# Kernel tuning notes

Hardware: AMD Instinct MI355X
Metric: run time of the kernel (lower is better)

## Reference

```python
import jax, jax.numpy as jnp
import numpy as np

NUM_NODES = 50000
NUM_GRAPHS = 50
HID = 128
GFD = 2
L = 4
EPS_MSG = 1e-7


def layer_norm(x, g, b, eps=1e-5):
    mu = jnp.mean(x, axis=-1, keepdims=True)
    xc = x - mu
    var = jnp.mean(xc * xc, axis=-1, keepdims=True)
    return xc * jax.lax.rsqrt(var + eps) * g + b


def gen_conv(x, src, dst, ea, t, W1, b1, g1, be1, W2, b2):
    # GENConv message: relu(x_j + edge_attr) + eps  -> [E, h]
    msg = jax.nn.relu(x[src] + ea) + EPS_MSG
    # per-destination, per-channel softmax weights of t*msg
    logits = msg * t
    m = jax.ops.segment_max(logits, dst, num_segments=NUM_NODES)
    m = jnp.where(jnp.isfinite(m), m, 0.0)  # isolated nodes -> -inf guard
    m = jax.lax.stop_gradient(m)
    ex = jnp.exp(logits - m[dst])
    s = jax.ops.segment_sum(ex, dst, num_segments=NUM_NODES)
    agg = jax.ops.segment_sum(ex * msg, dst, num_segments=NUM_NODES) / jnp.where(s > 0, s, 1.0)
    out = agg + x  # root residual inside GENConv
    # GENConv MLP: Linear(h,2h) -> LayerNorm -> ReLU -> Linear(2h,h)
    h = layer_norm(out @ W1 + b1, g1, be1)
    h = jax.nn.relu(h)
    return h @ W2 + b2


def forward(x, edge_index, edge_attr, graph_features, node_W, node_b, edge_W, edge_b,
            ts, W1s, b1s, g1s, be1s, W2s, b2s, ln_gs, ln_bs,
            head_W0, head_b0, head_W1, head_b1):
    src, dst = edge_index[0], edge_index[1]
    x = x @ node_W + node_b                 # node_encoder
    ea = edge_attr @ edge_W + edge_b        # edge_encoder
    # layers[0].conv applied directly (no pre-norm)
    x = gen_conv(x, src, dst, ea, ts[0], W1s[0], b1s[0], g1s[0], be1s[0], W2s[0], b2s[0])
    # remaining layers: res+ blocks: x = x + conv(act(norm(x)))
    for i in range(1, L):
        h = jax.nn.relu(layer_norm(x, ln_gs[i], ln_bs[i]))
        h = gen_conv(h, src, dst, ea, ts[i], W1s[i], b1s[i], g1s[i], be1s[i], W2s[i], b2s[i])
        x = x + h
    # final norm/act taken from layers[0]
    x = jax.nn.relu(layer_norm(x, ln_gs[0], ln_bs[0]))
    # dropout(p=0.1) is identity in eval mode
    # graph features broadcast to nodes (faithful reshape sequence)
    G = graph_features.shape[0]
    npg = x.shape[0] // G                   # nodes per graph
    t = jnp.repeat(graph_features.T[:, :, None], npg, axis=2)  # [gfd, G, npg]
    t = t.reshape(G, GFD, npg)              # row-major reinterpret (torch .view)
    t = jnp.transpose(t, (1, 0, 2)).reshape(GFD, G * npg)      # cat(unbind(0), dim=1)
    x = jnp.concatenate([x, t.T], axis=1)   # [N, h + gfd]
    x = jax.nn.relu(x @ head_W0 + head_b0)
    x = x @ head_W1 + head_b1
    return x


def setup_inputs() -> dict:
    key = jax.random.key(0)
    ks = jax.random.split(key, 32)
    E = 800000
    d_in, d_e = 64, 16

    def lin(k, fi, fo):
        return jax.random.normal(k, (fi, fo), jnp.float32) / np.sqrt(fi)

    inp = {
        'x': jax.random.normal(ks[0], (NUM_NODES, d_in), jnp.float32),
        'edge_index': jax.random.randint(ks[1], (2, E), 0, NUM_NODES, jnp.int64 if jax.config.jax_enable_x64 else jnp.int32),
        'edge_attr': jax.random.normal(ks[2], (E, d_e), jnp.float32),
        'graph_features': jax.random.normal(ks[3], (NUM_GRAPHS, GFD), jnp.float32),
        'node_W': lin(ks[4], d_in, HID), 'node_b': jnp.zeros((HID,), jnp.float32),
        'edge_W': lin(ks[5], d_e, HID), 'edge_b': jnp.zeros((HID,), jnp.float32),
        'ts': jnp.ones((L,), jnp.float32),
        'W1s': jnp.stack([lin(ks[6 + i], HID, 2 * HID) for i in range(L)]),
        'b1s': jnp.zeros((L, 2 * HID), jnp.float32),
        'g1s': jnp.ones((L, 2 * HID), jnp.float32),
        'be1s': jnp.zeros((L, 2 * HID), jnp.float32),
        'W2s': jnp.stack([lin(ks[10 + i], 2 * HID, HID) for i in range(L)]),
        'b2s': jnp.zeros((L, HID), jnp.float32),
        'ln_gs': jnp.ones((L, HID), jnp.float32),
        'ln_bs': jnp.zeros((L, HID), jnp.float32),
        'head_W0': lin(ks[14], HID + GFD, HID), 'head_b0': jnp.zeros((HID,), jnp.float32),
        'head_W1': lin(ks[15], HID, 1), 'head_b1': jnp.zeros((1,), jnp.float32),
    }
    return inp


def reference(x, edge_index, edge_attr, graph_features, node_W, node_b, edge_W, edge_b,
              ts, W1s, b1s, g1s, be1s, W2s, b2s, ln_gs, ln_bs,
              head_W0, head_b0, head_W1, head_b1):
    return forward(x, edge_index, edge_attr, graph_features, node_W, node_b, edge_W, edge_b,
                   ts, W1s, b1s, g1s, be1s, W2s, b2s, ln_gs, ln_bs,
                   head_W0, head_b0, head_W1, head_b1)
```

## Files before the change

### kernel.cpp

```cpp
#include <hip/hip_runtime.h>
#include <math.h>

#define EPS_MSG 1e-7f

typedef float v2f __attribute__((ext_vector_type(2)));
typedef float v4f __attribute__((ext_vector_type(4)));
typedef short bf16x8 __attribute__((ext_vector_type(8)));
typedef float f32x4 __attribute__((ext_vector_type(4)));
typedef unsigned short ush;

static __device__ inline v2f sp(float a) { v2f r; r.x = a; r.y = a; return r; }

__device__ inline unsigned short f2bf(float f) {
    union { float f; unsigned int i; } u; u.f = f;
    unsigned int b = u.i;
    return (unsigned short)((b + 0x7fffu + ((b >> 16) & 1u)) >> 16);
}
__device__ inline float bf2f(unsigned short h) {
    union { unsigned int i; float f; } u; u.i = ((unsigned int)h) << 16;
    return u.f;
}

__global__ void zero2_kernel(int* __restrict__ a, int* __restrict__ b, int n) {
    int i = blockIdx.x * 256 + threadIdx.x;
    if (i < n) { a[i] = 0; b[i] = 0; }
}

__global__ void deg_kernel(const int* __restrict__ ei, int* __restrict__ deg, int E) {
    int e = blockIdx.x * 256 + threadIdx.x;
    if (e < E) atomicAdd(&deg[ei[E + e]], 1);
}

__global__ __launch_bounds__(1024)
void scan1_kernel(const int* __restrict__ deg, int* __restrict__ offs,
                  int* __restrict__ bsum, int n) {
    __shared__ int sh[1024];
    int tid = threadIdx.x;
    int i = blockIdx.x * 1024 + tid;
    int v = (i < n) ? deg[i] : 0;
    sh[tid] = v;
    __syncthreads();
    for (int off = 1; off < 1024; off <<= 1) {
        int t = (tid >= off) ? sh[tid - off] : 0;
        __syncthreads();
        sh[tid] += t;
        __syncthreads();
    }
    if (i < n) offs[i] = sh[tid] - v;
    if (tid == 1023) bsum[blockIdx.x] = sh[tid];
}

__global__ __launch_bounds__(64)
void scan2_kernel(int* __restrict__ bsum, int nb) {
    int lane = threadIdx.x;
    int carry = 0;
    for (int base = 0; base < nb; base += 64) {
        int v = (base + lane < nb) ? bsum[base + lane] : 0;
        int incl = v;
#pragma unroll
        for (int off = 1; off < 64; off <<= 1) {
            int t = __shfl_up(incl, off, 64);
            if (lane >= off) incl += t;
        }
        if (base + lane < nb) bsum[base + lane] = incl - v + carry;
        carry += __shfl(incl, 63, 64);
    }
    if (lane == 0) bsum[nb] = carry;
}

__global__ void scan3_kernel(int* __restrict__ offs, const int* __restrict__ bsum, int n) {
    int i = blockIdx.x * 256 + threadIdx.x;
    if (i < n) offs[i] += bsum[i >> 10];
    else if (i == n) offs[n] = bsum[(n + 1023) >> 10];
}

__global__ void scatter_kernel(const int* __restrict__ ei, const float* __restrict__ edge_attr,
                               const int* __restrict__ offs, int* __restrict__ fill,
                               int* __restrict__ src_perm, float* __restrict__ attr_perm, int E) {
    int e = blockIdx.x * 256 + threadIdx.x;
    if (e >= E) return;
    int s = ei[e];
    int d = ei[E + e];
    int pos = offs[d] + atomicAdd(&fill[d], 1);
    src_perm[pos] = s;
    const float4* a = (const float4*)&edge_attr[(size_t)e * 16];
    float4* b = (float4*)&attr_perm[(size_t)pos * 16];
    b[0] = a[0]; b[1] = a[1]; b[2] = a[2]; b[3] = a[3];
}

__global__ void wswz_kernel(const float* __restrict__ W, unsigned short* __restrict__ WH,
                            unsigned short* __restrict__ WL, int K, int Ncol, int total) {
    int idx = blockIdx.x * 256 + threadIdx.x;
    if (idx >= total) return;
    int j = idx & 7;
    int lane = (idx >> 3) & 63;
    int rest = idx >> 9;
    int ks = K >> 5;
    int kstep = rest % ks;
    int rest2 = rest / ks;
    int nc = Ncol >> 4;
    int c16 = rest2 % nc;
    int l = rest2 / nc;
    int k = kstep * 32 + (lane >> 4) * 8 + j;
    int n = c16 * 16 + (lane & 15);
    float v = W[(size_t)l * K * Ncol + (size_t)k * Ncol + n];
    unsigned short hi = f2bf(v);
    unsigned short lo = f2bf(v - bf2f(hi));
    WH[idx] = hi;
    WL[idx] = lo;
}

__global__ __launch_bounds__(256)
void encode_kernel(const float* __restrict__ x, const float* __restrict__ W,
                   const float* __restrict__ b, float* __restrict__ out, int N) {
    __shared__ __align__(16) float Xa[32][64];
    int tid = threadIdx.x;
    int node0 = blockIdx.x * 32;
    {
        int row = tid >> 3;
        int col = (tid & 7) * 8;
        float4 v0 = make_float4(0, 0, 0, 0), v1 = make_float4(0, 0, 0, 0);
        if (node0 + row < N) {
            const float* sp_ = &x[(size_t)(node0 + row) * 64 + col];
            v0 = *(const float4*)sp_;
            v1 = *(const float4*)(sp_ + 4);
        }
        *(float4*)&Xa[row][col] = v0;
        *(float4*)&Xa[row][col + 4] = v1;
    }
    __syncthreads();
    int tx = tid & 31, rg = tid >> 5;
    int c = tx * 4;
    v2f ba = *(const v2f*)&b[c];
    v2f bb = *(const v2f*)&b[c + 2];
    v2f acc[4][2];
#pragma unroll
    for (int i = 0; i < 4; ++i) { acc[i][0] = ba; acc[i][1] = bb; }
    for (int k = 0; k < 64; k += 4) {
        v4f W0 = *(const v4f*)&W[(k + 0) * 128 + c];
        v4f W1r = *(const v4f*)&W[(k + 1) * 128 + c];
        v4f W2r = *(const v4f*)&W[(k + 2) * 128 + c];
        v4f W3r = *(const v4f*)&W[(k + 3) * 128 + c];
#pragma unroll
        for (int i = 0; i < 4; ++i) {
            v4f xv = *(const v4f*)&Xa[rg * 4 + i][k];
            acc[i][0] = __builtin_elementwise_fma(sp(xv.x), W0.xy, acc[i][0]);
            acc[i][1] = __builtin_elementwise_fma(sp(xv.x), W0.zw, acc[i][1]);
            acc[i][0] = __builtin_elementwise_fma(sp(xv.y), W1r.xy, acc[i][0]);
            acc[i][1] = __builtin_elementwise_fma(sp(xv.y), W1r.zw, acc[i][1]);
            acc[i][0] = __builtin_elementwise_fma(sp(xv.z), W2r.xy, acc[i][0]);
            acc[i][1] = __builtin_elementwise_fma(sp(xv.z), W2r.zw, acc[i][1]);
            acc[i][0] = __builtin_elementwise_fma(sp(xv.w), W3r.xy, acc[i][0]);
            acc[i][1] = __builtin_elementwise_fma(sp(xv.w), W3r.zw, acc[i][1]);
        }
    }
#pragma unroll
    for (int i = 0; i < 4; ++i) {
        int row = node0 + rg * 4 + i;
        if (row < N) {
            float4 o = make_float4(acc[i][0].x, acc[i][0].y, acc[i][1].x, acc[i][1].y);
            *(float4*)&out[(size_t)row * 128 + c] = o;
        }
    }
}

__global__ __launch_bounds__(256)
void ln_relu_kernel(const float* __restrict__ x, const float* __restrict__ g,
                    const float* __restrict__ b, float* __restrict__ out, int N) {
    int lane = threadIdx.x & 63;
    int node = blockIdx.x * 4 + (threadIdx.x >> 6);
    if (node >= N) return;
    int c0 = lane * 2;
    float2 xv = *(const float2*)&x[(size_t)node * 128 + c0];
    float s = xv.x + xv.y;
    float q = xv.x * xv.x + xv.y * xv.y;
#pragma unroll
    for (int m = 1; m < 64; m <<= 1) { s += __shfl_xor(s, m, 64); q += __shfl_xor(q, m, 64); }
    float mu = s * (1.f / 128.f);
    float var = q * (1.f / 128.f) - mu * mu;
    float rs = rsqrtf(var + 1e-5f);
    float ox = fmaxf((xv.x - mu) * rs * g[c0] + b[c0], 0.f);
    float oy = fmaxf((xv.y - mu) * rs * g[c0 + 1] + b[c0 + 1], 0.f);
    float2 o; o.x = ox; o.y = oy;
    *(float2*)&out[(size_t)node * 128 + c0] = o;
}

__global__ __launch_bounds__(256)
void ln_relu_bf_kernel(const float* __restrict__ x, const float* __restrict__ g,
                       const float* __restrict__ b, unsigned short* __restrict__ outH,
                       unsigned short* __restrict__ outL, int N) {
    int lane = threadIdx.x & 63;
    int node = blockIdx.x * 4 + (threadIdx.x >> 6);
    if (node >= N) return;
    int c0 = lane * 2;
    float2 xv = *(const float2*)&x[(size_t)node * 128 + c0];
    float s = xv.x + xv.y;
    float q = xv.x * xv.x + xv.y * xv.y;
#pragma unroll
    for (int m = 1; m < 64; m <<= 1) { s += __shfl_xor(s, m, 64); q += __shfl_xor(q, m, 64); }
    float mu = s * (1.f / 128.f);
    float var = q * (1.f / 128.f) - mu * mu;
    float rs = rsqrtf(var + 1e-5f);
    float ox = fmaxf((xv.x - mu) * rs * g[c0] + b[c0], 0.f);
    float oy = fmaxf((xv.y - mu) * rs * g[c0 + 1] + b[c0 + 1], 0.f);
    unsigned short hx = f2bf(ox), hy = f2bf(oy);
    unsigned short lx = f2bf(ox - bf2f(hx)), ly = f2bf(oy - bf2f(hy));
    *(unsigned int*)&outH[(size_t)node * 128 + c0] = (unsigned int)hx | ((unsigned int)hy << 16);
    *(unsigned int*)&outL[(size_t)node * 128 + c0] = (unsigned int)lx | ((unsigned int)ly << 16);
}

__global__ __launch_bounds__(256, 4)
void conv_kernel(const float* __restrict__ pre, const float* __restrict__ attr_perm,
                 const int* __restrict__ src_perm, const int* __restrict__ offs,
                 const float* __restrict__ edge_W, const float* __restrict__ edge_b,
                 const float* __restrict__ ts, int layer,
                 unsigned short* __restrict__ convH, unsigned short* __restrict__ convL, int N) {
    int lane = threadIdx.x & 63;
    int node = blockIdx.x * 4 + (threadIdx.x >> 6);
    if (node >= N) return;
    int c0 = lane * 2;
    v2f wE[16];
#pragma unroll
    for (int k = 0; k < 16; ++k) {
        wE[k].x = edge_W[k * 128 + c0];
        wE[k].y = edge_W[k * 128 + c0 + 1];
    }
    v2f eb; eb.x = edge_b[c0]; eb.y = edge_b[c0 + 1];
    float t = ts[layer];
    int i0 = offs[node], i1 = offs[node + 1];
    v2f xself = *(const v2f*)&pre[(size_t)node * 128 + c0];
    float sx = 0.f, sy = 0.f, wx = 0.f, wy = 0.f;
    int i = i0;
    for (; i + 3 < i1; i += 4) {
        int iu = __builtin_amdgcn_readfirstlane(i);
        int sn0 = src_perm[iu];
        int sn1 = src_perm[iu + 1];
        int sn2 = src_perm[iu + 2];
        int sn3 = src_perm[iu + 3];
        v2f x0 = *(const v2f*)&pre[(size_t)sn0 * 128 + c0];
        v2f x1 = *(const v2f*)&pre[(size_t)sn1 * 128 + c0];
        v2f x2 = *(const v2f*)&pre[(size_t)sn2 * 128 + c0];
        v2f x3 = *(const v2f*)&pre[(size_t)sn3 * 128 + c0];
        const v4f* ar = (const v4f*)(attr_perm + (size_t)iu * 16);
        v2f ea0 = eb, ea1 = eb, ea2 = eb, ea3 = eb;
#pragma unroll
        for (int k = 0; k < 4; ++k) {
            v4f A0 = ar[k];
            v4f A1 = ar[4 + k];
            v4f A2 = ar[8 + k];
            v4f A3 = ar[12 + k];
            ea0 = __builtin_elementwise_fma(sp(A0.x), wE[4 * k + 0], ea0);
            ea1 = __builtin_elementwise_fma(sp(A1.x), wE[4 * k + 0], ea1);
            ea2 = __builtin_elementwise_fma(sp(A2.x), wE[4 * k + 0], ea2);
            ea3 = __builtin_elementwise_fma(sp(A3.x), wE[4 * k + 0], ea3);
            ea0 = __builtin_elementwise_fma(sp(A0.y), wE[4 * k + 1], ea0);
            ea1 = __builtin_elementwise_fma(sp(A1.y), wE[4 * k + 1], ea1);
            ea2 = __builtin_elementwise_fma(sp(A2.y), wE[4 * k + 1], ea2);
            ea3 = __builtin_elementwise_fma(sp(A3.y), wE[4 * k + 1], ea3);
            ea0 = __builtin_elementwise_fma(sp(A0.z), wE[4 * k + 2], ea0);
            ea1 = __builtin_elementwise_fma(sp(A1.z), wE[4 * k + 2], ea1);
            ea2 = __builtin_elementwise_fma(sp(A2.z), wE[4 * k + 2], ea2);
            ea3 = __builtin_elementwise_fma(sp(A3.z), wE[4 * k + 2], ea3);
            ea0 = __builtin_elementwise_fma(sp(A0.w), wE[4 * k + 3], ea0);
            ea1 = __builtin_elementwise_fma(sp(A1.w), wE[4 * k + 3], ea1);
            ea2 = __builtin_elementwise_fma(sp(A2.w), wE[4 * k + 3], ea2);
            ea3 = __builtin_elementwise_fma(sp(A3.w), wE[4 * k + 3], ea3);
        }
        float m0x = fmaxf(x0.x + ea0.x, 0.f) + EPS_MSG;
        float m0y = fmaxf(x0.y + ea0.y, 0.f) + EPS_MSG;
        float m1x = fmaxf(x1.x + ea1.x, 0.f) + EPS_MSG;
        float m1y = fmaxf(x1.y + ea1.y, 0.f) + EPS_MSG;
        float m2x = fmaxf(x2.x + ea2.x, 0.f) + EPS_MSG;
        float m2y = fmaxf(x2.y + ea2.y, 0.f) + EPS_MSG;
        float m3x = fmaxf(x3.x + ea3.x, 0.f) + EPS_MSG;
        float m3y = fmaxf(x3.y + ea3.y, 0.f) + EPS_MSG;
        float e0x = __expf(m0x * t), e0y = __expf(m0y * t);
        float e1x = __expf(m1x * t), e1y = __expf(m1y * t);
        float e2x = __expf(m2x * t), e2y = __expf(m2y * t);
        float e3x = __expf(m3x * t), e3y = __expf(m3y * t);
        sx += (e0x + e1x) + (e2x + e3x);
        sy += (e0y + e1y) + (e2y + e3y);
        wx = fmaf(e0x, m0x, wx); wx = fmaf(e1x, m1x, wx);
        wx = fmaf(e2x, m2x, wx); wx = fmaf(e3x, m3x, wx);
        wy = fmaf(e0y, m0y, wy); wy = fmaf(e1y, m1y, wy);
        wy = fmaf(e2y, m2y, wy); wy = fmaf(e3y, m3y, wy);
    }
    for (; i < i1; ++i) {
        int iu = __builtin_amdgcn_readfirstlane(i);
        int sn = src_perm[iu];
        const v4f* ar = (const v4f*)(attr_perm + (size_t)iu * 16);
        v2f xv = *(const v2f*)&pre[(size_t)sn * 128 + c0];
        v2f ea = eb;
#pragma unroll
        for (int k = 0; k < 4; ++k) {
            v4f A0 = ar[k];
            ea = __builtin_elementwise_fma(sp(A0.x), wE[4 * k + 0], ea);
            ea = __builtin_elementwise_fma(sp(A0.y), wE[4 * k + 1], ea);
            ea = __builtin_elementwise_fma(sp(A0.z), wE[4 * k + 2], ea);
            ea = __builtin_elementwise_fma(sp(A0.w), wE[4 * k + 3], ea);
        }
        float mgx = fmaxf(xv.x + ea.x, 0.f) + EPS_MSG;
        float mgy = fmaxf(xv.y + ea.y, 0.f) + EPS_MSG;
        float ex = __expf(mgx * t), ey = __expf(mgy * t);
        sx += ex; sy += ey;
        wx = fmaf(ex, mgx, wx);
        wy = fmaf(ey, mgy, wy);
    }
    float ax = (sx > 0.f) ? wx / sx : 0.f;
    float ay = (sy > 0.f) ? wy / sy : 0.f;
    float ox = ax + xself.x;
    float oy = ay + xself.y;
    unsigned short hx = f2bf(ox), hy = f2bf(oy);
    unsigned short lx = f2bf(ox - bf2f(hx)), ly = f2bf(oy - bf2f(hy));
    *(unsigned int*)&convH[(size_t)node * 128 + c0] = (unsigned int)hx | ((unsigned int)hy << 16);
    *(unsigned int*)&convL[(size_t)node * 128 + c0] = (unsigned int)lx | ((unsigned int)ly << 16);
}

template <int RES>
__global__ __launch_bounds__(256)
void mlp_mfma(const unsigned short* __restrict__ convH, const unsigned short* __restrict__ convL,
              const unsigned short* __restrict__ W1H, const unsigned short* __restrict__ W1L,
              const float* __restrict__ b1, const float* __restrict__ g1, const float* __restrict__ be1,
              const unsigned short* __restrict__ W2H, const unsigned short* __restrict__ W2L,
              const float* __restrict__ b2, const float* __restrict__ xold,
              float* __restrict__ xnew, int N) {
    __shared__ __align__(16) char SH[33792];
    __shared__ float2 ps[4][32];
    ush (*XaH)[136] = (ush(*)[136])&SH[0];
    ush (*XaL)[136] = (ush(*)[136])&SH[8704];
    ush (*XhH)[264] = (ush(*)[264])&SH[0];
    ush (*XhL)[264] = (ush(*)[264])&SH[16896];
    int tid = threadIdx.x;
    int w = tid >> 6;
    int lane = tid & 63;
    int g = lane >> 4;
    int r = lane & 15;
    int node0 = blockIdx.x * 32;
    {
        int row = tid >> 3;
        int cb = (tid & 7) * 16;
        uint4 h0 = make_uint4(0, 0, 0, 0), h1 = h0, l0 = h0, l1 = h0;
        if (node0 + row < N) {
            const uint4* pH = (const uint4*)&convH[(size_t)(node0 + row) * 128 + cb];
            const uint4* pL = (const uint4*)&convL[(size_t)(node0 + row) * 128 + cb];
            h0 = pH[0]; h1 = pH[1];
            l0 = pL[0]; l1 = pL[1];
        }
        *(uint4*)&XaH[row][cb] = h0; *(uint4*)&XaH[row][cb + 8] = h1;
        *(uint4*)&XaL[row][cb] = l0; *(uint4*)&XaL[row][cb + 8] = l1;
    }
    __syncthreads();
    f32x4 acc1[2][4];
#pragma unroll
    for (int cf = 0; cf < 4; ++cf) {
        float bv = b1[(w * 4 + cf) * 16 + r];
        f32x4 iv; iv[0] = bv; iv[1] = bv; iv[2] = bv; iv[3] = bv;
        acc1[0][cf] = iv; acc1[1][cf] = iv;
    }
#pragma unroll
    for (int kstep = 0; kstep < 4; ++kstep) {
        int ko = kstep * 32 + g * 8;
        bf16x8 aH0 = *(const bf16x8*)&XaH[r][ko];
        bf16x8 aH1 = *(const bf16x8*)&XaH[16 + r][ko];
        bf16x8 aL0 = *(const bf16x8*)&XaL[r][ko];
        bf16x8 aL1 = *(const bf16x8*)&XaL[16 + r][ko];
#pragma unroll
        for (int cf = 0; cf < 4; ++cf) {
            int c16 = w * 4 + cf;
            bf16x8 bH = *(const bf16x8*)&W1H[(((size_t)c16 * 4 + kstep) * 64 + lane) * 8];
            bf16x8 bL = *(const bf16x8*)&W1L[(((size_t)c16 * 4 + kstep) * 64 + lane) * 8];
            acc1[0][cf] = __builtin_amdgcn_mfma_f32_16x16x32_bf16(aH0, bH, acc1[0][cf], 0, 0, 0);
            acc1[0][cf] = __builtin_amdgcn_mfma_f32_16x16x32_bf16(aH0, bL, acc1[0][cf], 0, 0, 0);
            acc1[0][cf] = __builtin_amdgcn_mfma_f32_16x16x32_bf16(aL0, bH, acc1[0][cf], 0, 0, 0);
            acc1[1][cf] = __builtin_amdgcn_mfma_f32_16x16x32_bf16(aH1, bH, acc1[1][cf], 0, 0, 0);
            acc1[1][cf] = __builtin_amdgcn_mfma_f32_16x16x32_bf16(aH1, bL, acc1[1][cf], 0, 0, 0);
            acc1[1][cf] = __builtin_amdgcn_mfma_f32_16x16x32_bf16(aL1, bH, acc1[1][cf], 0, 0, 0);
        }
    }
    {
        float s_[2][4], q_[2][4];
#pragma unroll
        for (int rf = 0; rf < 2; ++rf)
#pragma unroll
            for (int reg = 0; reg < 4; ++reg) {
                float s = 0.f, q = 0.f;
#pragma unroll
                for (int cf = 0; cf < 4; ++cf) {
                    float v = acc1[rf][cf][reg];
                    s += v; q += v * v;
                }
                s_[rf][reg] = s; q_[rf][reg] = q;
            }
#pragma unroll
        for (int m = 1; m < 16; m <<= 1) {
#pragma unroll
            for (int rf = 0; rf < 2; ++rf)
#pragma unroll
                for (int reg = 0; reg < 4; ++reg) {
                    s_[rf][reg] += __shfl_xor(s_[rf][reg], m, 64);
                    q_[rf][reg] += __shfl_xor(q_[rf][reg], m, 64);
                }
        }
        if (r == 0) {
#pragma unroll
            for (int rf = 0; rf < 2; ++rf)
#pragma unroll
                for (int reg = 0; reg < 4; ++reg)
                    ps[w][rf * 16 + g * 4 + reg] = make_float2(s_[rf][reg], q_[rf][reg]);
        }
    }
    __syncthreads();
    {
        float gv[4], bev[4];
#pragma unroll
        for (int cf = 0; cf < 4; ++cf) {
            gv[cf] = g1[(w * 4 + cf) * 16 + r];
            bev[cf] = be1[(w * 4 + cf) * 16 + r];
        }
#pragma unroll
        for (int rf = 0; rf < 2; ++rf)
#pragma unroll
            for (int reg = 0; reg < 4; ++reg) {
                int row = rf * 16 + g * 4 + reg;
                float2 t0 = ps[0][row], t1 = ps[1][row], t2 = ps[2][row], t3 = ps[3][row];
                float s = t0.x + t1.x + t2.x + t3.x;
                float q = t0.y + t1.y + t2.y + t3.y;
                float mu = s * (1.f / 256.f);
                float var = q * (1.f / 256.f) - mu * mu;
                float rs = rsqrtf(var + 1e-5f);
#pragma unroll
                for (int cf = 0; cf < 4; ++cf) {
                    float h = fmaxf((acc1[rf][cf][reg] - mu) * rs * gv[cf] + bev[cf], 0.f);
                    unsigned short hh = f2bf(h);
                    unsigned short hl = f2bf(h - bf2f(hh));
                    int col = (w * 4 + cf) * 16 + r;
                    XhH[row][col] = hh;
                    XhL[row][col] = hl;
                }
            }
    }
    __syncthreads();
    f32x4 acc2[2][2];
#pragma unroll
    for (int cf = 0; cf < 2; ++cf) {
        float bv = b2[(w * 2 + cf) * 16 + r];
        f32x4 iv; iv[0] = bv; iv[1] = bv; iv[2] = bv; iv[3] = bv;
        acc2[0][cf] = iv; acc2[1][cf] = iv;
    }
#pragma unroll
    for (int kstep = 0; kstep < 8; ++kstep) {
        int ko = kstep * 32 + g * 8;
        bf16x8 aH0 = *(const bf16x8*)&XhH[r][ko];
        bf16x8 aH1 = *(const bf16x8*)&XhH[16 + r][ko];
        bf16x8 aL0 = *(const bf16x8*)&XhL[r][ko];
        bf16x8 aL1 = *(const bf16x8*)&XhL[16 + r][ko];
#pragma unroll
        for (int cf = 0; cf < 2; ++cf) {
            int c16 = w * 2 + cf;
            bf16x8 bH = *(const bf16x8*)&W2H[(((size_t)c16 * 8 + kstep) * 64 + lane) * 8];
            bf16x8 bL = *(const bf16x8*)&W2L[(((size_t)c16 * 8 + kstep) * 64 + lane) * 8];
            acc2[0][cf] = __builtin_amdgcn_mfma_f32_16x16x32_bf16(aH0, bH, acc2[0][cf], 0, 0, 0);
            acc2[0][cf] = __builtin_amdgcn_mfma_f32_16x16x32_bf16(aH0, bL, acc2[0][cf], 0, 0, 0);
            acc2[0][cf] = __builtin_amdgcn_mfma_f32_16x16x32_bf16(aL0, bH, acc2[0][cf], 0, 0, 0);
            acc2[1][cf] = __builtin_amdgcn_mfma_f32_16x16x32_bf16(aH1, bH, acc2[1][cf], 0, 0, 0);
            acc2[1][cf] = __builtin_amdgcn_mfma_f32_16x16x32_bf16(aH1, bL, acc2[1][cf], 0, 0, 0);
            acc2[1][cf] = __builtin_amdgcn_mfma_f32_16x16x32_bf16(aL1, bH, acc2[1][cf], 0, 0, 0);
        }
    }
#pragma unroll
    for (int rf = 0; rf < 2; ++rf)
#pragma unroll
        for (int reg = 0; reg < 4; ++reg) {
            int row = node0 + rf * 16 + g * 4 + reg;
            if (row < N) {
#pragma unroll
                for (int cf = 0; cf < 2; ++cf) {
                    int col = (w * 2 + cf) * 16 + r;
                    float v = acc2[rf][cf][reg];
                    if (RES) v += xold[(size_t)row * 128 + col];
                    xnew[(size_t)row * 128 + col] = v;
                }
            }
        }
}

__global__ __launch_bounds__(256)
void head_mfma(const unsigned short* __restrict__ PREH, const unsigned short* __restrict__ PREL,
               const unsigned short* __restrict__ W0H, const unsigned short* __restrict__ W0L,
               const float* __restrict__ W0, const float* __restrict__ b0,
               const float* __restrict__ gf, const float* __restrict__ W1h,
               const float* __restrict__ b1h, float* __restrict__ out, int N) {
    __shared__ __align__(16) unsigned short XH[32][136];
    __shared__ __align__(16) unsigned short XL[32][136];
    __shared__ float gf0s[32], gf1s[32];
    __shared__ float psum[4][32];
    int tid = threadIdx.x;
    int w = tid >> 6;
    int lane = tid & 63;
    int g = lane >> 4;
    int r = lane & 15;
    int node0 = blockIdx.x * 32;
    {
        int row = tid >> 3;
        int cb = (tid & 7) * 16;
        uint4 h0 = make_uint4(0, 0, 0, 0), h1 = h0, l0 = h0, l1 = h0;
        if (node0 + row < N) {
            const uint4* pH = (const uint4*)&PREH[(size_t)(node0 + row) * 128 + cb];
            const uint4* pL = (const uint4*)&PREL[(size_t)(node0 + row) * 128 + cb];
            h0 = pH[0]; h1 = pH[1];
            l0 = pL[0]; l1 = pL[1];
        }
        *(uint4*)&XH[row][cb] = h0; *(uint4*)&XH[row][cb + 8] = h1;
        *(uint4*)&XL[row][cb] = l0; *(uint4*)&XL[row][cb + 8] = l1;
        if (tid < 32) {
            int node = node0 + tid;
            float f0 = 0.f, f1 = 0.f;
            if (node < N) {
                int a = node / 1000;
                int i0 = 2 * a, i1 = 2 * a + 1;
                f0 = (i0 < 50) ? gf[i0 * 2] : gf[(i0 - 50) * 2 + 1];
                f1 = (i1 < 50) ? gf[i1 * 2] : gf[(i1 - 50) * 2 + 1];
            }
            gf0s[tid] = f0;
            gf1s[tid] = f1;
        }
    }
    __syncthreads();
    f32x4 acc[2][2];
#pragma unroll
    for (int cf = 0; cf < 2; ++cf) {
        float bv = b0[(w * 2 + cf) * 16 + r];
        f32x4 iv; iv[0] = bv; iv[1] = bv; iv[2] = bv; iv[3] = bv;
        acc[0][cf] = iv; acc[1][cf] = iv;
    }
#pragma unroll
    for (int kstep = 0; kstep < 4; ++kstep) {
        int ko = kstep * 32 + g * 8;
        bf16x8 aH0 = *(const bf16x8*)&XH[r][ko];
        bf16x8 aH1 = *(const bf16x8*)&XH[16 + r][ko];
        bf16x8 aL0 = *(const bf16x8*)&XL[r][ko];
        bf16x8 aL1 = *(const bf16x8*)&XL[16 + r][ko];
#pragma unroll
        for (int cf = 0; cf < 2; ++cf) {
            int c16 = w * 2 + cf;
            bf16x8 bH = *(const bf16x8*)&W0H[(((size_t)c16 * 4 + kstep) * 64 + lane) * 8];
            bf16x8 bL = *(const bf16x8*)&W0L[(((size_t)c16 * 4 + kstep) * 64 + lane) * 8];
            acc[0][cf] = __builtin_amdgcn_mfma_f32_16x16x32_bf16(aH0, bH, acc[0][cf], 0, 0, 0);
            acc[0][cf] = __builtin_amdgcn_mfma_f32_16x16x32_bf16(aH0, bL, acc[0][cf], 0, 0, 0);
            acc[0][cf] = __builtin_amdgcn_mfma_f32_16x16x32_bf16(aL0, bH, acc[0][cf], 0, 0, 0);
            acc[1][cf] = __builtin_amdgcn_mfma_f32_16x16x32_bf16(aH1, bH, acc[1][cf], 0, 0, 0);
            acc[1][cf] = __builtin_amdgcn_mfma_f32_16x16x32_bf16(aH1, bL, acc[1][cf], 0, 0, 0);
            acc[1][cf] = __builtin_amdgcn_mfma_f32_16x16x32_bf16(aL1, bH, acc[1][cf], 0, 0, 0);
        }
    }
    {
        float w1v[2], wg0[2], wg1[2];
#pragma unroll
        for (int cf = 0; cf < 2; ++cf) {
            int col = (w * 2 + cf) * 16 + r;
            w1v[cf] = W1h[col];
            wg0[cf] = W0[128 * 128 + col];
            wg1[cf] = W0[129 * 128 + col];
        }
#pragma unroll
        for (int rf = 0; rf < 2; ++rf)
#pragma unroll
            for (int reg = 0; reg < 4; ++reg) {
                int rowl = rf * 16 + g * 4 + reg;
                float f0 = gf0s[rowl], f1 = gf1s[rowl];
                float p = 0.f;
#pragma unroll
                for (int cf = 0; cf < 2; ++cf) {
                    float v = acc[rf][cf][reg] + f0 * wg0[cf] + f1 * wg1[cf];
                    v = fmaxf(v, 0.f);
                    p = fmaf(v, w1v[cf], p);
                }
#pragma unroll
                for (int m = 1; m < 16; m <<= 1) p += __shfl_xor(p, m, 64);
                if (r == 0) psum[w][rowl] = p;
            }
    }
    __syncthreads();
    if (tid < 32) {
        int node = node0 + tid;
        if (node < N) {
            float s = psum[0][tid] + psum[1][tid] + psum[2][tid] + psum[3][tid] + b1h[0];
            out[node] = s;
        }
    }
}

extern "C" void kernel_launch(void* const* d_in, const int* in_sizes, int n_in,
                              void* d_out, int out_size, void* d_ws, size_t ws_size,
                              hipStream_t stream) {
    const float* x_in    = (const float*)d_in[0];
    const int*   ei      = (const int*)d_in[1];
    const float* edge_attr = (const float*)d_in[2];
    const float* gf      = (const float*)d_in[3];
    const float* node_W  = (const float*)d_in[4];
    const float* node_b  = (const float*)d_in[5];
    const float* edge_W  = (const float*)d_in[6];
    const float* edge_b  = (const float*)d_in[7];
    const float* ts      = (const float*)d_in[8];
    const float* W1s     = (const float*)d_in[9];
    const float* b1s     = (const float*)d_in[10];
    const float* g1s     = (const float*)d_in[11];
    const float* be1s    = (const float*)d_in[12];
    const float* W2s     = (const float*)d_in[13];
    const float* b2s     = (const float*)d_in[14];
    const float* ln_gs   = (const float*)d_in[15];
    const float* ln_bs   = (const float*)d_in[16];
    const float* hW0     = (const float*)d_in[17];
    const float* hb0     = (const float*)d_in[18];
    const float* hW1     = (const float*)d_in[19];
    const float* hb1     = (const float*)d_in[20];

    const int N = in_sizes[0] / 64;
    const int E = in_sizes[1] / 2;
    const int NB = (N + 1023) / 1024;

    char* ws = (char*)d_ws;
    size_t off = 0;
    auto alloc = [&](size_t bytes) -> void* {
        void* p = ws + off;
        off = (off + bytes + 255) & ~(size_t)255;
        return p;
    };
    float* X     = (float*)alloc((size_t)N * 128 * 4);
    float* PRE   = (float*)alloc((size_t)N * 128 * 4);
    unsigned short* CONVH = (unsigned short*)alloc((size_t)N * 128 * 2);
    unsigned short* CONVL = (unsigned short*)alloc((size_t)N * 128 * 2);
    unsigned short* W1H = (unsigned short*)alloc((size_t)4 * 128 * 256 * 2);
    unsigned short* W1L = (unsigned short*)alloc((size_t)4 * 128 * 256 * 2);
    unsigned short* W2H = (unsigned short*)alloc((size_t)4 * 256 * 128 * 2);
    unsigned short* W2L = (unsigned short*)alloc((size_t)4 * 256 * 128 * 2);
    int* SRCP    = (int*)alloc((size_t)E * 4);
    int* DEG     = (int*)alloc((size_t)N * 4);
    int* FILL    = (int*)alloc((size_t)N * 4);
    int* OFFS    = (int*)alloc((size_t)(N + 1) * 4);
    int* BSUM    = (int*)alloc((size_t)(NB + 1) * 4);
    float* ATTRP = (float*)alloc((size_t)E * 16 * 4);

    unsigned short* W0H = (unsigned short*)DEG;
    unsigned short* W0L = W0H + 128 * 128;

    const int TOT = 4 * 128 * 256;
    wswz_kernel<<<(TOT + 255) / 256, 256, 0, stream>>>(W1s, W1H, W1L, 128, 256, TOT);
    wswz_kernel<<<(TOT + 255) / 256, 256, 0, stream>>>(W2s, W2H, W2L, 256, 128, TOT);

    zero2_kernel<<<(N + 255) / 256, 256, 0, stream>>>(DEG, FILL, N);
    deg_kernel<<<(E + 255) / 256, 256, 0, stream>>>(ei, DEG, E);
    scan1_kernel<<<NB, 1024, 0, stream>>>(DEG, OFFS, BSUM, N);
    scan2_kernel<<<1, 64, 0, stream>>>(BSUM, NB);
    scan3_kernel<<<(N + 256) / 256, 256, 0, stream>>>(OFFS, BSUM, N);
    scatter_kernel<<<(E + 255) / 256, 256, 0, stream>>>(ei, edge_attr, OFFS, FILL, SRCP, ATTRP, E);
    wswz_kernel<<<(128 * 128 + 255) / 256, 256, 0, stream>>>(hW0, W0H, W0L, 128, 128, 128 * 128);

    encode_kernel<<<(N + 31) / 32, 256, 0, stream>>>(x_in, node_W, node_b, X, N);

    for (int layer = 0; layer < 4; ++layer) {
        const float* pre = X;
        if (layer > 0) {
            ln_relu_kernel<<<(N + 3) / 4, 256, 0, stream>>>(X, ln_gs + 128 * layer, ln_bs + 128 * layer, PRE, N);
            pre = PRE;
        }
        conv_kernel<<<(N + 3) / 4, 256, 0, stream>>>(pre, ATTRP, SRCP, OFFS, edge_W, edge_b,
                                                     ts, layer, CONVH, CONVL, N);
        const unsigned short* w1h = W1H + (size_t)layer * 128 * 256;
        const unsigned short* w1l = W1L + (size_t)layer * 128 * 256;
        const unsigned short* w2h = W2H + (size_t)layer * 256 * 128;
        const unsigned short* w2l = W2L + (size_t)layer * 256 * 128;
        if (layer == 0)
            mlp_mfma<0><<<(N + 31) / 32, 256, 0, stream>>>(CONVH, CONVL, w1h, w1l,
                                                           b1s + layer * 256, g1s + layer * 256, be1s + layer * 256,
                                                           w2h, w2l, b2s + layer * 128, X, X, N);
        else
            mlp_mfma<1><<<(N + 31) / 32, 256, 0, stream>>>(CONVH, CONVL, w1h, w1l,
                                                           b1s + layer * 256, g1s + layer * 256, be1s + layer * 256,
                                                           w2h, w2l, b2s + layer * 128, X, X, N);
    }

    ln_relu_bf_kernel<<<(N + 3) / 4, 256, 0, stream>>>(X, ln_gs, ln_bs, CONVH, CONVL, N);
    head_mfma<<<(N + 31) / 32, 256, 0, stream>>>(CONVH, CONVL, W0H, W0L, hW0, hb0, gf, hW1, hb1,
                                                 (float*)d_out, N);
}
```

Measured before the change: 662.7 us.

## Gather neighbor features from a bf16 copy and split edge-attr permutation into gather

Encoder and per-layer LayerNorm+ReLU kernels now also write a bf16 copy of node features. The conv kernel reads neighbor features from that copy, halving the bytes of the random per-edge gather. The scatter kernel now records only edge ids, and a separate coalesced gather kernel permutes edge attributes. The bf16 path reduces message precision, risks tolerance failures, and is used only when the workspace has room.

```diff
diff --git a/kernel.cpp b/kernel.cpp
--- a/kernel.cpp
+++ b/kernel.cpp
@@ -19,6 +19,11 @@
 __device__ inline float bf2f(unsigned short h) {
     union { unsigned int i; float f; } u; u.i = ((unsigned int)h) << 16;
     return u.f;
+}
+__device__ inline v2f ubf2(unsigned int u) {
+    union { unsigned int i; float f; } a, b;
+    a.i = u << 16; b.i = u & 0xffff0000u;
+    v2f r; r.x = a.f; r.y = b.f; return r;
 }
 
 __global__ void zero2_kernel(int* __restrict__ a, int* __restrict__ b, int n) {
@@ -74,18 +79,27 @@
     else if (i == n) offs[n] = bsum[(n + 1023) >> 10];
 }
 
-__global__ void scatter_kernel(const int* __restrict__ ei, const float* __restrict__ edge_attr,
-                               const int* __restrict__ offs, int* __restrict__ fill,
-                               int* __restrict__ src_perm, float* __restrict__ attr_perm, int E) {
+__global__ void scatter_pos_kernel(const int* __restrict__ ei, const int* __restrict__ offs,
+                                   int* __restrict__ fill, int* __restrict__ src_perm,
+                                   int* __restrict__ eid_perm, int E) {
     int e = blockIdx.x * 256 + threadIdx.x;
     if (e >= E) return;
     int s = ei[e];
     int d = ei[E + e];
     int pos = offs[d] + atomicAdd(&fill[d], 1);
     src_perm[pos] = s;
-    const float4* a = (const float4*)&edge_attr[(size_t)e * 16];
-    float4* b = (float4*)&attr_perm[(size_t)pos * 16];
-    b[0] = a[0]; b[1] = a[1]; b[2] = a[2]; b[3] = a[3];
+    eid_perm[pos] = e;
+}
+
+__global__ void gather_attr_kernel(const float* __restrict__ edge_attr,
+                                   const int* __restrict__ eid_perm,
+                                   float* __restrict__ attr_perm, int E) {
+    int idx = blockIdx.x * 256 + threadIdx.x;
+    if (idx >= E * 4) return;
+    int p = idx >> 2, c = idx & 3;
+    int e = eid_perm[p];
+    float4 v = *(const float4*)&edge_attr[(size_t)e * 16 + c * 4];
+    *(float4*)&attr_perm[(size_t)p * 16 + c * 4] = v;
 }
 
 __global__ void wswz_kernel(const float* __restrict__ W, unsigned short* __restrict__ WH,
@@ -112,7 +126,8 @@
 
 __global__ __launch_bounds__(256)
 void encode_kernel(const float* __restrict__ x, const float* __restrict__ W,
-                   const float* __restrict__ b, float* __restrict__ out, int N) {
+                   const float* __restrict__ b, float* __restrict__ out,
+                   unsigned short* __restrict__ xb, int N) {
     __shared__ __align__(16) float Xa[32][64];
     int tid = threadIdx.x;
     int node0 = blockIdx.x * 32;
@@ -160,13 +175,20 @@
         if (row < N) {
             float4 o = make_float4(acc[i][0].x, acc[i][0].y, acc[i][1].x, acc[i][1].y);
             *(float4*)&out[(size_t)row * 128 + c] = o;
+            if (xb) {
+                unsigned int u0 = (unsigned int)f2bf(o.x) | ((unsigned int)f2bf(o.y) << 16);
+                unsigned int u1 = (unsigned int)f2bf(o.z) | ((unsigned int)f2bf(o.w) << 16);
+                *(unsigned int*)&xb[(size_t)row * 128 + c] = u0;
+                *(unsigned int*)&xb[(size_t)row * 128 + c + 2] = u1;
+            }
         }
     }
 }
 
 __global__ __launch_bounds__(256)
 void ln_relu_kernel(const float* __restrict__ x, const float* __restrict__ g,
-                    const float* __restrict__ b, float* __restrict__ out, int N) {
+                    const float* __restrict__ b, float* __restrict__ out,
+                    unsigned short* __restrict__ gb, int N) {
     int lane = threadIdx.x & 63;
     int node = blockIdx.x * 4 + (threadIdx.x >> 6);
     if (node >= N) return;
@@ -183,6 +205,10 @@
     float oy = fmaxf((xv.y - mu) * rs * g[c0 + 1] + b[c0 + 1], 0.f);
     float2 o; o.x = ox; o.y = oy;
     *(float2*)&out[(size_t)node * 128 + c0] = o;
+    if (gb) {
+        unsigned int u = (unsigned int)f2bf(ox) | ((unsigned int)f2bf(oy) << 16);
+        *(unsigned int*)&gb[(size_t)node * 128 + c0] = u;
+    }
 }
 
 __global__ __launch_bounds__(256)
@@ -209,8 +235,10 @@
     *(unsigned int*)&outL[(size_t)node * 128 + c0] = (unsigned int)lx | ((unsigned int)ly << 16);
 }
 
+template <int BF>
 __global__ __launch_bounds__(256, 4)
-void conv_kernel(const float* __restrict__ pre, const float* __restrict__ attr_perm,
+void conv_kernel(const float* __restrict__ pre, const unsigned short* __restrict__ preb,
+                 const float* __restrict__ attr_perm,
                  const int* __restrict__ src_perm, const int* __restrict__ offs,
                  const float* __restrict__ edge_W, const float* __restrict__ edge_b,
                  const float* __restrict__ ts, int layer,
@@ -237,10 +265,19 @@
         int sn1 = src_perm[iu + 1];
         int sn2 = src_perm[iu + 2];
         int sn3 = src_perm[iu + 3];
-        v2f x0 = *(const v2f*)&pre[(size_t)sn0 * 128 + c0];
-        v2f x1 = *(const v2f*)&pre[(size_t)sn1 * 128 + c0];
-        v2f x2 = *(const v2f*)&pre[(size_t)sn2 * 128 + c0];
-        v2f x3 = *(const v2f*)&pre[(size_t)sn3 * 128 + c0];
+        v2f x0, x1, x2, x3;
+        if (BF) {
+            unsigned int u0 = *(const unsigned int*)&preb[(size_t)sn0 * 128 + c0];
+            unsigned int u1 = *(const unsigned int*)&preb[(size_t)sn1 * 128 + c0];
+            unsigned int u2 = *(const unsigned int*)&preb[(size_t)sn2 * 128 + c0];
+            unsigned int u3 = *(const unsigned int*)&preb[(size_t)sn3 * 128 + c0];
+            x0 = ubf2(u0); x1 = ubf2(u1); x2 = ubf2(u2); x3 = ubf2(u3);
+        } else {
+            x0 = *(const v2f*)&pre[(size_t)sn0 * 128 + c0];
+            x1 = *(const v2f*)&pre[(size_t)sn1 * 128 + c0];
+            x2 = *(const v2f*)&pre[(size_t)sn2 * 128 + c0];
+            x3 = *(const v2f*)&pre[(size_t)sn3 * 128 + c0];
+        }
         const v4f* ar = (const v4f*)(attr_perm + (size_t)iu * 16);
         v2f ea0 = eb, ea1 = eb, ea2 = eb, ea3 = eb;
 #pragma unroll
@@ -289,7 +326,13 @@
         int iu = __builtin_amdgcn_readfirstlane(i);
         int sn = src_perm[iu];
         const v4f* ar = (const v4f*)(attr_perm + (size_t)iu * 16);
-        v2f xv = *(const v2f*)&pre[(size_t)sn * 128 + c0];
+        v2f xv;
+        if (BF) {
+            unsigned int u = *(const unsigned int*)&preb[(size_t)sn * 128 + c0];
+            xv = ubf2(u);
+        } else {
+            xv = *(const v2f*)&pre[(size_t)sn * 128 + c0];
+        }
         v2f ea = eb;
 #pragma unroll
         for (int k = 0; k < 4; ++k) {
@@ -641,8 +684,13 @@
     int* BSUM    = (int*)alloc((size_t)(NB + 1) * 4);
     float* ATTRP = (float*)alloc((size_t)E * 16 * 4);
 
+    unsigned short* GB = (unsigned short*)(ws + off);
+    int mode_bf = (off + (size_t)N * 128 * 2 <= ws_size) ? 1 : 0;
+    if (!mode_bf) GB = nullptr;
+
     unsigned short* W0H = (unsigned short*)DEG;
     unsigned short* W0L = W0H + 128 * 128;
+    int* EIDP = (int*)CONVH;
 
     const int TOT = 4 * 128 * 256;
     wswz_kernel<<<(TOT + 255) / 256, 256, 0, stream>>>(W1s, W1H, W1L, 128, 256, TOT);
@@ -653,19 +701,25 @@
     scan1_kernel<<<NB, 1024, 0, stream>>>(DEG, OFFS, BSUM, N);
     scan2_kernel<<<1, 64, 0, stream>>>(BSUM, NB);
     scan3_kernel<<<(N + 256) / 256, 256, 0, stream>>>(OFFS, BSUM, N);
-    scatter_kernel<<<(E + 255) / 256, 256, 0, stream>>>(ei, edge_attr, OFFS, FILL, SRCP, ATTRP, E);
+    scatter_pos_kernel<<<(E + 255) / 256, 256, 0, stream>>>(ei, OFFS, FILL, SRCP, EIDP, E);
+    gather_attr_kernel<<<(E * 4 + 255) / 256, 256, 0, stream>>>(edge_attr, EIDP, ATTRP, E);
     wswz_kernel<<<(128 * 128 + 255) / 256, 256, 0, stream>>>(hW0, W0H, W0L, 128, 128, 128 * 128);
 
-    encode_kernel<<<(N + 31) / 32, 256, 0, stream>>>(x_in, node_W, node_b, X, N);
+    encode_kernel<<<(N + 31) / 32, 256, 0, stream>>>(x_in, node_W, node_b, X, GB, N);
 
     for (int layer = 0; layer < 4; ++layer) {
         const float* pre = X;
         if (layer > 0) {
-            ln_relu_kernel<<<(N + 3) / 4, 256, 0, stream>>>(X, ln_gs + 128 * layer, ln_bs + 128 * layer, PRE, N);
+            ln_relu_kernel<<<(N + 3) / 4, 256, 0, stream>>>(X, ln_gs + 128 * layer, ln_bs + 128 * layer,
+                                                            PRE, GB, N);
             pre = PRE;
         }
-        conv_kernel<<<(N + 3) / 4, 256, 0, stream>>>(pre, ATTRP, SRCP, OFFS, edge_W, edge_b,
-                                                     ts, layer, CONVH, CONVL, N);
+        if (mode_bf)
+            conv_kernel<1><<<(N + 3) / 4, 256, 0, stream>>>(pre, GB, ATTRP, SRCP, OFFS, edge_W, edge_b,
+                                                            ts, layer, CONVH, CONVL, N);
+        else
+            conv_kernel<0><<<(N + 3) / 4, 256, 0, stream>>>(pre, nullptr, ATTRP, SRCP, OFFS, edge_W, edge_b,
+                                                            ts, layer, CONVH, CONVL, N);
         const unsigned short* w1h = W1H + (size_t)layer * 128 * 256;
         const unsigned short* w1l = W1L + (size_t)layer * 128 * 256;
         const unsigned short* w2h = W2H + (size_t)layer * 256 * 128;
```

Result: no change. 674.2 us (+1.7%).
